# Kernel optimization log

Measured on AMD Instinct MI355X. Metric: run time of the kernel, lower is better.

The kernel has to match this reference:

```python
import jax, jax.numpy as jnp
import numpy as np

# Module hyperparameters (init_kwargs)
IN_CHANNELS = 16
N_SEGMENTS = 32
LOGSIG_DEPTH = 2  # depth-2 log-signature: level1 increments + Levy areas
LOGSIG_CHANNELS = IN_CHANNELS + IN_CHANNELS * (IN_CHANNELS - 1) // 2  # 136

N_BATCHS = 8
BATCH_SIZE = 16
NT = 2048


def setup_inputs() -> dict:
    key = jax.random.key(0)
    k1, k2 = jax.random.split(key)
    inp = jax.random.normal(k1, (N_BATCHS * BATCH_SIZE, NT, IN_CHANNELS), dtype=jnp.float32)
    # lengths >= 2*n_segments so the repeat-padding branch of the torch code is never taken
    length = jax.random.randint(k2, (N_BATCHS,), 256, NT + 1)
    return {"inp": inp, "length": length, "n_batchs": N_BATCHS}


def _gather_time(arr, idx):
    # arr: [B, nT, ...], idx: [B, K] -> [B, K, ...]
    B, nT = arr.shape[0], arr.shape[1]
    trail = arr.shape[2:]
    flat = arr.reshape(B, nT, -1)
    idx_b = jnp.broadcast_to(idx[:, :, None], (B, idx.shape[1], flat.shape[-1]))
    out = jnp.take_along_axis(flat, idx_b, axis=1)
    return out.reshape(B, idx.shape[1], *trail)


def reference(inp, length, n_batchs):
    # Depth-2 log-signature over N_SEGMENTS variable-length windows per group.
    # Level 1: window increment x_b - x_a.
    # Level 2 (Lyndon words i<j): Levy area A_ij = 0.5 * sum_{l in [a,b)} [(x_l - x_a)_i dx_l_j - (x_l - x_a)_j dx_l_i]
    # computed from a prefix sum P_t = sum_{l<t} (x_l ^ dx_l) gathered at segment boundaries.
    B, nT, d = inp.shape
    batch_size = B // n_batchs
    S = N_SEGMENTS

    dx = inp[:, 1:] - inp[:, :-1]                              # [B, nT-1, d]
    c = jnp.einsum('bti,btj->btij', inp[:, :-1], dx)
    c = c - jnp.swapaxes(c, -1, -2)                            # antisymmetric outer products
    P = jnp.concatenate(
        [jnp.zeros((B, 1, d, d), inp.dtype), jnp.cumsum(c, axis=1)], axis=1
    )                                                          # [B, nT, d, d], P_t = sum_{l<t} c_l

    # boundary point indices per group: t_vec = round(linspace(1, L, S+1)), 0-based
    frac = jnp.arange(S + 1, dtype=jnp.float32) / S
    Lf = length.astype(jnp.float32)[:, None]
    tv = jnp.round(1.0 + (Lf - 1.0) * frac[None, :]).astype(jnp.int32) - 1  # [n_batchs, S+1]
    idx = jnp.repeat(tv, batch_size, axis=0)                   # [B, S+1]

    xb = _gather_time(inp, idx)                                # [B, S+1, d]
    Pb = _gather_time(P, idx)                                  # [B, S+1, d, d]

    xa, xe = xb[:, :-1], xb[:, 1:]
    lvl1 = xe - xa                                             # [B, S, d]
    corr = jnp.einsum('bsi,bsj->bsij', xa, lvl1)
    corr = corr - jnp.swapaxes(corr, -1, -2)
    A = 0.5 * (Pb[:, 1:] - Pb[:, :-1] - corr)                  # [B, S, d, d] Levy areas
    iu, ju = jnp.triu_indices(d, k=1)
    lvl2 = A[:, :, iu, ju]                                     # [B, S, d(d-1)/2]
    return jnp.concatenate([lvl1, lvl2], axis=-1)              # [B, S, LOGSIG_CHANNELS]
```

## Files before the change

### kernel.cpp

```cpp
#include <hip/hip_runtime.h>

#define NT    2048
#define D     16
#define NSEG  32
#define NOUTC 136

typedef __attribute__((ext_vector_type(8))) short bf16x8;
typedef __attribute__((ext_vector_type(4))) float f32x4;

__global__ __launch_bounds__(64) void logsig_kernel(
    const float* __restrict__ inp,
    const int*   __restrict__ length,
    float*       __restrict__ out,
    int batch_size)
{
    const int blk  = blockIdx.x;
    const int b    = blk / NSEG;
    const int s    = blk % NSEG;
    const int g    = b / batch_size;
    const int lane = threadIdx.x;

    __shared__ float xT[D * 68];
    __shared__ float Cs[16 * 17];

    const float Lm1 = __fadd_rn((float)length[g], -1.0f);
    const int t0 = (int)rintf(__fadd_rn(1.0f, __fmul_rn(Lm1, (float)s       * (1.0f/32.0f)))) - 1;
    const int t1 = (int)rintf(__fadd_rn(1.0f, __fmul_rn(Lm1, (float)(s + 1) * (1.0f/32.0f)))) - 1;
    const int n  = t1 - t0;

    const float* xrow = inp + (size_t)b * NT * D;
    const float4* src = (const float4*)(xrow + (size_t)t0 * D);

    const int nvec = (n + 1) * 4;
    for (int v = lane; v < nvec; v += 64) {
        const float4 q = src[v];
        const int t  = v >> 2;
        const int c4 = (v & 3) << 2;
        xT[(c4 + 0) * 68 + t] = q.x;
        xT[(c4 + 1) * 68 + t] = q.y;
        xT[(c4 + 2) * 68 + t] = q.z;
        xT[(c4 + 3) * 68 + t] = q.w;
    }
    __syncthreads();

    const int ch = lane & 15;
    const int tb = lane >> 4;
    const float* base = &xT[ch * 68];

    f32x4 acc = {0.f, 0.f, 0.f, 0.f};
    const int nchunks = (n > 32) ? 2 : 1;

    for (int c = 0; c < nchunks; ++c) {
        const int kb = c * 32 + 8 * tb;
        const f32x4 q0 = *(const f32x4*)(base + kb);
        const f32x4 q1 = *(const f32x4*)(base + kb + 4);
        const float x9 = base[kb + 8];
        float xv[9] = {q0[0], q0[1], q0[2], q0[3], q1[0], q1[1], q1[2], q1[3], x9};

        bf16x8 Ah, Al, Bh, Bl;
        #pragma unroll
        for (int e = 0; e < 8; ++e) {
            const int idx = kb + e;
            const float xm  = (idx <= n) ? xv[e] : 0.0f;
            const float dxm = (idx <  n) ? (xv[e + 1] - xv[e]) : 0.0f;
            const unsigned bx = __float_as_uint(xm);
            Ah[e] = (short)(bx >> 16);
            const float lx = xm - __uint_as_float(bx & 0xFFFF0000u);
            Al[e] = (short)(__float_as_uint(lx) >> 16);
            const unsigned bd = __float_as_uint(dxm);
            Bh[e] = (short)(bd >> 16);
            const float ld = dxm - __uint_as_float(bd & 0xFFFF0000u);
            Bl[e] = (short)(__float_as_uint(ld) >> 16);
        }
        acc = __builtin_amdgcn_mfma_f32_16x16x32_bf16(Ah, Bh, acc, 0, 0, 0);
        acc = __builtin_amdgcn_mfma_f32_16x16x32_bf16(Ah, Bl, acc, 0, 0, 0);
        acc = __builtin_amdgcn_mfma_f32_16x16x32_bf16(Al, Bh, acc, 0, 0, 0);
    }

    #pragma unroll
    for (int e = 0; e < 4; ++e)
        Cs[(4 * tb + e) * 17 + ch] = acc[e];
    __syncthreads();

    const float xa_j = base[0];
    const float xe_j = base[n];
    const size_t obase = ((size_t)b * NSEG + s) * NOUTC;

    if (tb == 0) {
        out[obase + ch] = xe_j - xa_j;
    }
    #pragma unroll
    for (int e = 0; e < 4; ++e) {
        const int i = 4 * tb + e;
        const int j = ch;
        if (i < j) {
            const float Mt   = Cs[j * 17 + i];
            const float xa_i = xT[i * 68 + 0];
            const float xe_i = xT[i * 68 + n];
            const float corr = xa_i * (xe_j - xa_j) - xa_j * (xe_i - xa_i);
            const int oidx   = 15 * i - (i * (i - 1)) / 2 + (j - i - 1);
            out[obase + D + oidx] = 0.5f * (acc[e] - Mt - corr);
        }
    }
}

extern "C" void kernel_launch(void* const* d_in, const int* in_sizes, int n_in,
                              void* d_out, int out_size, void* d_ws, size_t ws_size,
                              hipStream_t stream)
{
    const float* inp    = (const float*)d_in[0];
    const int*   length = (const int*)d_in[1];
    float*       out    = (float*)d_out;

    const int B  = in_sizes[0] / (NT * D);
    const int G  = in_sizes[1];
    const int bs = B / G;

    const int grid = B * NSEG;
    logsig_kernel<<<grid, 64, 0, stream>>>(inp, length, out, bs);
}
```

Before: 9.929 us.

## Split segment K-chunks across two waves and unroll global loads

```diff
diff --git a/kernel.cpp b/kernel.cpp
--- a/kernel.cpp
+++ b/kernel.cpp
@@ -8,7 +8,7 @@
 typedef __attribute__((ext_vector_type(8))) short bf16x8;
 typedef __attribute__((ext_vector_type(4))) float f32x4;
 
-__global__ __launch_bounds__(64) void logsig_kernel(
+__global__ __launch_bounds__(128) void logsig_kernel(
     const float* __restrict__ inp,
     const int*   __restrict__ length,
     float*       __restrict__ out,
@@ -18,10 +18,12 @@
     const int b    = blk / NSEG;
     const int s    = blk % NSEG;
     const int g    = b / batch_size;
-    const int lane = threadIdx.x;
+    const int tid  = threadIdx.x;
+    const int wave = tid >> 6;
+    const int lane = tid & 63;
 
     __shared__ float xT[D * 68];
-    __shared__ float Cs[16 * 17];
+    __shared__ float Cs[2][16 * 17];
 
     const float Lm1 = __fadd_rn((float)length[g], -1.0f);
     const int t0 = (int)rintf(__fadd_rn(1.0f, __fmul_rn(Lm1, (float)s       * (1.0f/32.0f)))) - 1;
@@ -32,14 +34,25 @@
     const float4* src = (const float4*)(xrow + (size_t)t0 * D);
 
     const int nvec = (n + 1) * 4;
-    for (int v = lane; v < nvec; v += 64) {
-        const float4 q = src[v];
-        const int t  = v >> 2;
-        const int c4 = (v & 3) << 2;
-        xT[(c4 + 0) * 68 + t] = q.x;
-        xT[(c4 + 1) * 68 + t] = q.y;
-        xT[(c4 + 2) * 68 + t] = q.z;
-        xT[(c4 + 3) * 68 + t] = q.w;
+    const int v0 = tid, v1 = tid + 128, v2 = tid + 256;
+    const float4 q0 = src[min(v0, nvec - 1)];
+    const float4 q1 = src[min(v1, nvec - 1)];
+    const float4 q2 = src[min(v2, nvec - 1)];
+
+    if (v0 < nvec) {
+        const int t = v0 >> 2, c4 = (v0 & 3) << 2;
+        xT[(c4 + 0) * 68 + t] = q0.x; xT[(c4 + 1) * 68 + t] = q0.y;
+        xT[(c4 + 2) * 68 + t] = q0.z; xT[(c4 + 3) * 68 + t] = q0.w;
+    }
+    if (v1 < nvec) {
+        const int t = v1 >> 2, c4 = (v1 & 3) << 2;
+        xT[(c4 + 0) * 68 + t] = q1.x; xT[(c4 + 1) * 68 + t] = q1.y;
+        xT[(c4 + 2) * 68 + t] = q1.z; xT[(c4 + 3) * 68 + t] = q1.w;
+    }
+    if (v2 < nvec) {
+        const int t = v2 >> 2, c4 = (v2 & 3) << 2;
+        xT[(c4 + 0) * 68 + t] = q2.x; xT[(c4 + 1) * 68 + t] = q2.y;
+        xT[(c4 + 2) * 68 + t] = q2.z; xT[(c4 + 3) * 68 + t] = q2.w;
     }
     __syncthreads();
 
@@ -48,14 +61,12 @@
     const float* base = &xT[ch * 68];
 
     f32x4 acc = {0.f, 0.f, 0.f, 0.f};
-    const int nchunks = (n > 32) ? 2 : 1;
-
-    for (int c = 0; c < nchunks; ++c) {
-        const int kb = c * 32 + 8 * tb;
-        const f32x4 q0 = *(const f32x4*)(base + kb);
-        const f32x4 q1 = *(const f32x4*)(base + kb + 4);
+    if (wave == 0 || n > 32) {
+        const int kb = wave * 32 + 8 * tb;
+        const f32x4 p0 = *(const f32x4*)(base + kb);
+        const f32x4 p1 = *(const f32x4*)(base + kb + 4);
         const float x9 = base[kb + 8];
-        float xv[9] = {q0[0], q0[1], q0[2], q0[3], q1[0], q1[1], q1[2], q1[3], x9};
+        float xv[9] = {p0[0], p0[1], p0[2], p0[3], p1[0], p1[1], p1[2], p1[3], x9};
 
         bf16x8 Ah, Al, Bh, Bl;
         #pragma unroll
@@ -79,28 +90,23 @@
 
     #pragma unroll
     for (int e = 0; e < 4; ++e)
-        Cs[(4 * tb + e) * 17 + ch] = acc[e];
+        Cs[wave][(4 * tb + e) * 17 + ch] = acc[e];
     __syncthreads();
 
-    const float xa_j = base[0];
-    const float xe_j = base[n];
     const size_t obase = ((size_t)b * NSEG + s) * NOUTC;
-
-    if (tb == 0) {
-        out[obase + ch] = xe_j - xa_j;
+    if (tid < D) {
+        out[obase + tid] = xT[tid * 68 + n] - xT[tid * 68];
     }
-    #pragma unroll
-    for (int e = 0; e < 4; ++e) {
-        const int i = 4 * tb + e;
-        const int j = ch;
-        if (i < j) {
-            const float Mt   = Cs[j * 17 + i];
-            const float xa_i = xT[i * 68 + 0];
-            const float xe_i = xT[i * 68 + n];
-            const float corr = xa_i * (xe_j - xa_j) - xa_j * (xe_i - xa_i);
-            const int oidx   = 15 * i - (i * (i - 1)) / 2 + (j - i - 1);
-            out[obase + D + oidx] = 0.5f * (acc[e] - Mt - corr);
-        }
+    if (tid < 120) {
+        int p = tid, i = 0;
+        while (i < D - 2 && p >= (D - 1 - i)) { p -= (D - 1 - i); ++i; }
+        const int j = i + 1 + p;
+        const float Mij = Cs[0][i * 17 + j] + Cs[1][i * 17 + j];
+        const float Mji = Cs[0][j * 17 + i] + Cs[1][j * 17 + i];
+        const float xai = xT[i * 68],     xei = xT[i * 68 + n];
+        const float xaj = xT[j * 68],     xej = xT[j * 68 + n];
+        const float corr = xai * (xej - xaj) - xaj * (xei - xai);
+        out[obase + D + tid] = 0.5f * (Mij - Mji - corr);
     }
 }
 
@@ -117,5 +123,5 @@
     const int bs = B / G;
 
     const int grid = B * NSEG;
-    logsig_kernel<<<grid, 64, 0, stream>>>(inp, length, out, bs);
+    logsig_kernel<<<grid, 128, 0, stream>>>(inp, length, out, bs);
 }
```

Result: slower. 12.10 us (+21.9%).

## Pack four segments per block, load directly from global, coalesce output writes

Applied to the files above, without the earlier changes.

```diff
diff --git a/kernel.cpp b/kernel.cpp
--- a/kernel.cpp
+++ b/kernel.cpp
@@ -8,55 +8,70 @@
 typedef __attribute__((ext_vector_type(8))) short bf16x8;
 typedef __attribute__((ext_vector_type(4))) float f32x4;
 
-__global__ __launch_bounds__(64) void logsig_kernel(
+__device__ const unsigned char PAIR_TAB[120] = {
+    0x01,0x02,0x03,0x04,0x05,0x06,0x07,0x08,0x09,0x0A,0x0B,0x0C,0x0D,0x0E,0x0F,
+    0x12,0x13,0x14,0x15,0x16,0x17,0x18,0x19,0x1A,0x1B,0x1C,0x1D,0x1E,0x1F,
+    0x23,0x24,0x25,0x26,0x27,0x28,0x29,0x2A,0x2B,0x2C,0x2D,0x2E,0x2F,
+    0x34,0x35,0x36,0x37,0x38,0x39,0x3A,0x3B,0x3C,0x3D,0x3E,0x3F,
+    0x45,0x46,0x47,0x48,0x49,0x4A,0x4B,0x4C,0x4D,0x4E,0x4F,
+    0x56,0x57,0x58,0x59,0x5A,0x5B,0x5C,0x5D,0x5E,0x5F,
+    0x67,0x68,0x69,0x6A,0x6B,0x6C,0x6D,0x6E,0x6F,
+    0x78,0x79,0x7A,0x7B,0x7C,0x7D,0x7E,0x7F,
+    0x89,0x8A,0x8B,0x8C,0x8D,0x8E,0x8F,
+    0x9A,0x9B,0x9C,0x9D,0x9E,0x9F,
+    0xAB,0xAC,0xAD,0xAE,0xAF,
+    0xBC,0xBD,0xBE,0xBF,
+    0xCD,0xCE,0xCF,
+    0xDE,0xDF,
+    0xEF
+};
+
+__global__ __launch_bounds__(256) void logsig_kernel(
     const float* __restrict__ inp,
     const int*   __restrict__ length,
     float*       __restrict__ out,
     int batch_size)
 {
     const int blk  = blockIdx.x;
-    const int b    = blk / NSEG;
-    const int s    = blk % NSEG;
+    const int b    = blk >> 3;
+    const int sq   = blk & 7;
+    const int tid  = threadIdx.x;
+    const int wave = tid >> 6;
+    const int lane = tid & 63;
+    const int s    = sq * 4 + wave;
     const int g    = b / batch_size;
-    const int lane = threadIdx.x;
 
-    __shared__ float xT[D * 68];
-    __shared__ float Cs[16 * 17];
+    __shared__ float slab[4][16 * 17 + 32];
+    float* Cs   = slab[wave];
+    float* xa_s = Cs + 272;
+    float* xe_s = Cs + 288;
 
     const float Lm1 = __fadd_rn((float)length[g], -1.0f);
     const int t0 = (int)rintf(__fadd_rn(1.0f, __fmul_rn(Lm1, (float)s       * (1.0f/32.0f)))) - 1;
     const int t1 = (int)rintf(__fadd_rn(1.0f, __fmul_rn(Lm1, (float)(s + 1) * (1.0f/32.0f)))) - 1;
     const int n  = t1 - t0;
 
-    const float* xrow = inp + (size_t)b * NT * D;
-    const float4* src = (const float4*)(xrow + (size_t)t0 * D);
-
-    const int nvec = (n + 1) * 4;
-    for (int v = lane; v < nvec; v += 64) {
-        const float4 q = src[v];
-        const int t  = v >> 2;
-        const int c4 = (v & 3) << 2;
-        xT[(c4 + 0) * 68 + t] = q.x;
-        xT[(c4 + 1) * 68 + t] = q.y;
-        xT[(c4 + 2) * 68 + t] = q.z;
-        xT[(c4 + 3) * 68 + t] = q.w;
-    }
-    __syncthreads();
+    const float* xrow = inp + (size_t)b * (NT * D);
 
     const int ch = lane & 15;
     const int tb = lane >> 4;
-    const float* base = &xT[ch * 68];
+
+    if (lane < D) {
+        xa_s[lane] = xrow[t0 * D + lane];
+        xe_s[lane] = xrow[t1 * D + lane];
+    }
 
     f32x4 acc = {0.f, 0.f, 0.f, 0.f};
-    const int nchunks = (n > 32) ? 2 : 1;
-
-    for (int c = 0; c < nchunks; ++c) {
+    const int nch = (n > 32) ? 2 : 1;
+    for (int c = 0; c < nch; ++c) {
         const int kb = c * 32 + 8 * tb;
-        const f32x4 q0 = *(const f32x4*)(base + kb);
-        const f32x4 q1 = *(const f32x4*)(base + kb + 4);
-        const float x9 = base[kb + 8];
-        float xv[9] = {q0[0], q0[1], q0[2], q0[3], q1[0], q1[1], q1[2], q1[3], x9};
-
+        float xv[9];
+        #pragma unroll
+        for (int e = 0; e < 9; ++e) {
+            int t = t0 + kb + e;
+            t = (t < NT - 1) ? t : (NT - 1);
+            xv[e] = xrow[t * D + ch];
+        }
         bf16x8 Ah, Al, Bh, Bl;
         #pragma unroll
         for (int e = 0; e < 8; ++e) {
@@ -82,25 +97,22 @@
         Cs[(4 * tb + e) * 17 + ch] = acc[e];
     __syncthreads();
 
-    const float xa_j = base[0];
-    const float xe_j = base[n];
     const size_t obase = ((size_t)b * NSEG + s) * NOUTC;
-
-    if (tb == 0) {
-        out[obase + ch] = xe_j - xa_j;
-    }
-    #pragma unroll
-    for (int e = 0; e < 4; ++e) {
-        const int i = 4 * tb + e;
-        const int j = ch;
-        if (i < j) {
-            const float Mt   = Cs[j * 17 + i];
-            const float xa_i = xT[i * 68 + 0];
-            const float xe_i = xT[i * 68 + n];
-            const float corr = xa_i * (xe_j - xa_j) - xa_j * (xe_i - xa_i);
-            const int oidx   = 15 * i - (i * (i - 1)) / 2 + (j - i - 1);
-            out[obase + D + oidx] = 0.5f * (acc[e] - Mt - corr);
+    for (int o = lane; o < NOUTC; o += 64) {
+        float val;
+        if (o < D) {
+            val = xe_s[o] - xa_s[o];
+        } else {
+            const int pc = PAIR_TAB[o - D];
+            const int i = pc >> 4, j = pc & 15;
+            const float Mij = Cs[i * 17 + j];
+            const float Mji = Cs[j * 17 + i];
+            const float xai = xa_s[i], xaj = xa_s[j];
+            const float xei = xe_s[i], xej = xe_s[j];
+            const float corr = xai * (xej - xaj) - xaj * (xei - xai);
+            val = 0.5f * (Mij - Mji - corr);
         }
+        out[obase + o] = val;
     }
 }
 
@@ -116,6 +128,6 @@
     const int G  = in_sizes[1];
     const int bs = B / G;
 
-    const int grid = B * NSEG;
-    logsig_kernel<<<grid, 64, 0, stream>>>(inp, length, out, bs);
+    const int grid = B * (NSEG / 4);
+    logsig_kernel<<<grid, 256, 0, stream>>>(inp, length, out, bs);
 }
```

Result: no change. 9.869 us (-0.6%).
